# Performance work log

Measured on AMD Instinct MI355X. Metric: run time of the kernel, lower is better.

Reference implementation:

```python
import jax, jax.numpy as jnp
import numpy as np

V, D, T, H = 32000, 1024, 1024, 16
HD = D // H  # head_size = 64
B = 4


def setup_inputs() -> dict:
    key = jax.random.key(0)
    ks = jax.random.split(key, 12)
    s = 0.02
    return {
        "idx": jax.random.randint(ks[0], (B, T), 0, V),
        "tok_emb": jax.random.normal(ks[1], (V, D), jnp.float32) * s,
        "pos_emb": jax.random.normal(ks[2], (T, D), jnp.float32) * s,
        "Wq": jax.random.normal(ks[3], (H, D, HD), jnp.float32) * s,
        "Wk": jax.random.normal(ks[4], (H, D, HD), jnp.float32) * s,
        "Wv": jax.random.normal(ks[5], (H, D, HD), jnp.float32) * s,
        "W1": jax.random.normal(ks[6], (D, D), jnp.float32) * s,
        "b1": jnp.zeros((D,), jnp.float32),
        "W2": jax.random.normal(ks[7], (D, D), jnp.float32) * s,
        "b2": jnp.zeros((D,), jnp.float32),
        "Wout": jax.random.normal(ks[8], (D, V), jnp.float32) * s,
        "bout": jnp.zeros((V,), jnp.float32),
    }


def reference(idx, tok_emb, pos_emb, Wq, Wk, Wv, W1, b1, W2, b2, Wout, bout):
    t = idx.shape[1]
    x = tok_emb[idx] + pos_emb[:t]  # [B,T,D]
    # per-head q,k,v projections (no bias), vectorized over heads
    q = jnp.einsum("btd,hde->bhte", x, Wq)
    k = jnp.einsum("btd,hde->bhte", x, Wk)
    v = jnp.einsum("btd,hde->bhte", x, Wv)
    scores = jnp.einsum("bhte,bhse->bhts", q, k) / jnp.sqrt(jnp.float32(HD))
    causal = jnp.tril(jnp.ones((t, t), bool))
    scores = jnp.where(causal, scores, -jnp.inf)
    w = jax.nn.softmax(scores, axis=-1)
    att = jnp.einsum("bhts,bhse->bhte", w, v)  # [B,H,T,HD]
    # concat heads along feature dim -> [B,T,D]
    out = att.transpose(0, 2, 1, 3).reshape(idx.shape[0], t, D)
    h = jax.nn.relu(out @ W1 + b1)
    h = jax.nn.relu(h @ W2 + b2)
    logits = h @ Wout + bout  # [B,T,V]
    return logits
```

## Files before the change

kernel.cpp:

```cpp
#include <hip/hip_runtime.h>
#include <cstdint>
#include <cstddef>


#define DEV __device__ __forceinline__

typedef __attribute__((ext_vector_type(8))) short bf16x8;
typedef __attribute__((ext_vector_type(4))) float f32x4;

DEV unsigned short f2bf(float f) {
  unsigned u = __float_as_uint(f);
  u = (u + 0x7fffu + ((u >> 16) & 1u)) >> 16;
  return (unsigned short)u;
}

DEV void stage16(const void* g, void* l) {
  __builtin_amdgcn_global_load_lds(
      (const __attribute__((address_space(1))) unsigned int*)g,
      (__attribute__((address_space(3))) unsigned int*)l, 16, 0, 0);
}

__global__ __launch_bounds__(256) void k_embed(
    const int* __restrict__ idx, const float* __restrict__ tok,
    const float* __restrict__ pos, unsigned short* __restrict__ xb) {
  int i = blockIdx.x * 256 + threadIdx.x;
  int row = i >> 8;
  int c4 = i & 255;
  int t = row & 1023;
  int tokid = idx[row];
  const float4 a = ((const float4*)tok)[(size_t)tokid * 256 + c4];
  const float4 p = ((const float4*)pos)[(size_t)t * 256 + c4];
  ushort4 o;
  o.x = f2bf(a.x + p.x); o.y = f2bf(a.y + p.y);
  o.z = f2bf(a.z + p.z); o.w = f2bf(a.w + p.w);
  ((ushort4*)xb)[i] = o;
}

__global__ __launch_bounds__(256) void k_pack_qkv(
    const float* __restrict__ Wq, const float* __restrict__ Wk,
    const float* __restrict__ Wv, unsigned short* __restrict__ out) {
  __shared__ float tile[64][65];
  int blk = blockIdx.x;
  int p = blk >> 8, h = (blk >> 4) & 15, d0 = (blk & 15) * 64;
  const float* W = (p == 0) ? Wq : ((p == 1) ? Wk : Wv);
  int tid = threadIdx.x, rq = tid >> 6, cc = tid & 63;
#pragma unroll
  for (int it = 0; it < 16; ++it) {
    int dr = it * 4 + rq;
    tile[dr][cc] = W[((size_t)h * 1024 + d0 + dr) * 64 + cc];
  }
  __syncthreads();
#pragma unroll
  for (int it = 0; it < 16; ++it) {
    int e = it * 4 + rq;
    out[((size_t)(p * 1024 + h * 64 + e)) * 1024 + d0 + cc] = f2bf(tile[cc][e]);
  }
}

__global__ __launch_bounds__(256) void k_transpose(
    const float* __restrict__ in, unsigned short* __restrict__ out,
    int R, int C) {
  __shared__ float tile[64][65];
  int c0 = blockIdx.x * 64, r0 = blockIdx.y * 64;
  int tid = threadIdx.x, rq = tid >> 6, cc = tid & 63;
#pragma unroll
  for (int it = 0; it < 16; ++it) {
    int r = it * 4 + rq;
    tile[r][cc] = in[(size_t)(r0 + r) * C + c0 + cc];
  }
  __syncthreads();
#pragma unroll
  for (int it = 0; it < 16; ++it) {
    int c = it * 4 + rq;
    out[(size_t)(c0 + c) * R + r0 + cc] = f2bf(tile[cc][c]);
  }
}

template <int EP>
__global__ __launch_bounds__(256) void k_gemm(
    const unsigned short* __restrict__ A, const unsigned short* __restrict__ Bt,
    const float* __restrict__ bias, void* __restrict__ out0,
    void* __restrict__ out1, void* __restrict__ out2, int M, int N, int K) {
  __shared__ __align__(16) unsigned short As[128 * 32];
  __shared__ __align__(16) unsigned short Bs[128 * 32];
  const int tid = threadIdx.x;
  const int lane = tid & 63, w = tid >> 6;
  const int wr = w >> 1, wc = w & 1;
  const int fr = lane & 15, fg = lane >> 4;
  const int m0 = blockIdx.y * 128, n0 = blockIdx.x * 128;
  const int pch = (fg ^ ((fr >> 1) & 3)) << 3;

  f32x4 zero = {0.f, 0.f, 0.f, 0.f};
  f32x4 acc[4][4];
#pragma unroll
  for (int m = 0; m < 4; ++m)
#pragma unroll
    for (int n = 0; n < 4; ++n) acc[m][n] = zero;

  const int srow = tid >> 2;
  const int sch = (((tid & 3) ^ ((srow >> 1) & 3))) * 8;
  const unsigned short* Ab0 = A + (size_t)(m0 + srow) * K + sch;
  const unsigned short* Ab1 = A + (size_t)(m0 + 64 + srow) * K + sch;
  const unsigned short* Bb0 = Bt + (size_t)(n0 + srow) * K + sch;
  const unsigned short* Bb1 = Bt + (size_t)(n0 + 64 + srow) * K + sch;
  unsigned short* Ad0 = &As[tid * 8];
  unsigned short* Ad1 = &As[(tid + 256) * 8];
  unsigned short* Bd0 = &Bs[tid * 8];
  unsigned short* Bd1 = &Bs[(tid + 256) * 8];

  for (int k0 = 0; k0 < K; k0 += 32) {
    stage16(Ab0 + k0, Ad0);
    stage16(Ab1 + k0, Ad1);
    stage16(Bb0 + k0, Bd0);
    stage16(Bb1 + k0, Bd1);
    __syncthreads();
    bf16x8 af[4], bfv[4];
#pragma unroll
    for (int m = 0; m < 4; ++m)
      af[m] = *(const bf16x8*)&As[(wr * 64 + m * 16 + fr) * 32 + pch];
#pragma unroll
    for (int n = 0; n < 4; ++n)
      bfv[n] = *(const bf16x8*)&Bs[(wc * 64 + n * 16 + fr) * 32 + pch];
#pragma unroll
    for (int m = 0; m < 4; ++m)
#pragma unroll
      for (int n = 0; n < 4; ++n)
        acc[m][n] = __builtin_amdgcn_mfma_f32_16x16x32_bf16(af[m], bfv[n],
                                                            acc[m][n], 0, 0, 0);
    __syncthreads();
  }

#pragma unroll
  for (int m = 0; m < 4; ++m) {
#pragma unroll
    for (int n = 0; n < 4; ++n) {
      const int rb = m0 + wr * 64 + m * 16 + fg * 4;
      const int cc = n0 + wc * 64 + n * 16 + fr;
#pragma unroll
      for (int i = 0; i < 4; ++i) {
        float v = acc[m][n][i];
        const int r = rb + i;
        if (EP == 1) {
          v += bias[cc];
          v = v > 0.f ? v : 0.f;
          ((unsigned short*)out0)[(size_t)r * N + cc] = f2bf(v);
        } else if (EP == 3) {
          int p = cc >> 10, rem = cc & 1023;
          int h = rem >> 6, e = rem & 63;
          int b = r >> 10, t = r & 1023;
          unsigned short* dst =
              (p == 0) ? (unsigned short*)out0
                       : ((p == 1) ? (unsigned short*)out1 : (unsigned short*)out2);
          dst[(((size_t)(b * 16 + h) * 1024) + t) * 64 + e] = f2bf(v);
        }
      }
    }
  }
}

__global__ __launch_bounds__(512, 2) void k_gemm256(
    const unsigned short* __restrict__ A, const unsigned short* __restrict__ Bt,
    const float* __restrict__ bias, float* __restrict__ out,
    int M, int N, int K) {
  __shared__ __align__(16) unsigned short sm[4 * 16384];
  const int tid = threadIdx.x;
  const int lane = tid & 63, wid = tid >> 6;
  const int wr = wid >> 2, wc = wid & 3;
  const int fr = lane & 15, fg = lane >> 4;
  const int pch = (fg ^ ((fr >> 1) & 3)) << 3;

  const int nwg = gridDim.x * gridDim.y;
  int wg = blockIdx.y * gridDim.x + blockIdx.x;
  if ((nwg & 7) == 0) wg = (wg & 7) * (nwg >> 3) + (wg >> 3);
  const int m0 = (wg % gridDim.y) * 256;
  const int n0 = (wg / gridDim.y) * 256;

  const int srow = tid >> 2;
  const int scol = (((tid & 3) ^ ((srow >> 1) & 3))) * 8;
  const int NT = K >> 5;

#define STAGE_A(t, bb)                                                      \
  do {                                                                      \
    const unsigned short* g = A + (size_t)(m0 + srow) * K + (t) * 32 + scol; \
    stage16(g, &sm[(bb) * 16384 + tid * 8]);                                \
    stage16(g + (size_t)128 * K, &sm[(bb) * 16384 + 4096 + tid * 8]);       \
  } while (0)
#define STAGE_B(t, bb)                                                      \
  do {                                                                      \
    const unsigned short* g = Bt + (size_t)(n0 + srow) * K + (t) * 32 + scol; \
    stage16(g, &sm[(bb) * 16384 + 8192 + tid * 8]);                         \
    stage16(g + (size_t)128 * K, &sm[(bb) * 16384 + 8192 + 4096 + tid * 8]); \
  } while (0)

#define RD_G0(dA, dB, base)                                                 \
  do {                                                                      \
    _Pragma("unroll") for (int m_ = 0; m_ < 4; ++m_)                        \
      dA[m_] = *(const bf16x8*)&(base)[(wr * 128 + m_ * 16 + fr) * 32 + pch]; \
    _Pragma("unroll") for (int n_ = 0; n_ < 4; ++n_)                        \
      dB[n_] = *(const bf16x8*)&(base)[8192 + (wc * 64 + n_ * 16 + fr) * 32 + pch]; \
  } while (0)
#define RD_AHI(dA, base)                                                    \
  do {                                                                      \
    _Pragma("unroll") for (int m_ = 0; m_ < 4; ++m_)                        \
      dA[m_] = *(const bf16x8*)&(base)[(wr * 128 + (m_ + 4) * 16 + fr) * 32 + pch]; \
  } while (0)

#define MFMA_G(rbase, a, b)                                                 \
  do {                                                                      \
    __builtin_amdgcn_s_setprio(1);                                          \
    _Pragma("unroll") for (int m_ = 0; m_ < 4; ++m_)                        \
    _Pragma("unroll") for (int n_ = 0; n_ < 4; ++n_)                        \
      acc[(rbase) + m_][n_] = __builtin_amdgcn_mfma_f32_16x16x32_bf16(      \
          a[m_], b[n_], acc[(rbase) + m_][n_], 0, 0, 0);                    \
    __builtin_amdgcn_s_setprio(0);                                          \
  } while (0)

#define TILE_BODY(t, curA, curB, nxtA, nxtB)                                \
  do {                                                                      \
    const unsigned short* Ab_ = &sm[((t) & 3) * 16384];                     \
    bf16x8 a1_[4];                                                          \
    RD_AHI(a1_, Ab_);                                                       \
    if ((t) + 3 < NT) STAGE_A((t) + 3, ((t) + 3) & 3);                      \
    MFMA_G(0, curA, curB);                                                  \
    if ((t) + 1 < NT) {                                                     \
      const unsigned short* An_ = &sm[(((t) + 1) & 3) * 16384];             \
      RD_G0(nxtA, nxtB, An_);                                               \
    }                                                                       \
    if ((t) + 3 < NT) STAGE_B((t) + 3, ((t) + 3) & 3);                      \
    MFMA_G(4, a1_, curB);                                                   \
    if ((t) + 3 < NT) {                                                     \
      asm volatile("s_waitcnt vmcnt(4)" ::: "memory");                      \
    } else {                                                                \
      asm volatile("s_waitcnt vmcnt(0)" ::: "memory");                      \
    }                                                                       \
    __builtin_amdgcn_s_barrier();                                           \
  } while (0)

  f32x4 zero = {0.f, 0.f, 0.f, 0.f};
  f32x4 acc[8][4];
#pragma unroll
  for (int m = 0; m < 8; ++m)
#pragma unroll
    for (int n = 0; n < 4; ++n) acc[m][n] = zero;

  STAGE_A(0, 0); STAGE_B(0, 0);
  STAGE_A(1, 1); STAGE_B(1, 1);
  STAGE_A(2, 2); STAGE_B(2, 2);
  asm volatile("s_waitcnt vmcnt(4)" ::: "memory");
  __builtin_amdgcn_s_barrier();

  bf16x8 xA[4], xB[4], yA[4], yB[4];
  RD_G0(xA, xB, &sm[0]);

  for (int t = 0; t < NT; t += 2) {
    TILE_BODY(t, xA, xB, yA, yB);
    TILE_BODY(t + 1, yA, yB, xA, xB);
  }
#undef STAGE_A
#undef STAGE_B
#undef RD_G0
#undef RD_AHI
#undef MFMA_G
#undef TILE_BODY

#pragma unroll
  for (int m = 0; m < 8; ++m) {
#pragma unroll
    for (int n = 0; n < 4; ++n) {
      const int rb = m0 + wr * 128 + m * 16 + fg * 4;
      const int cc = n0 + wc * 64 + n * 16 + fr;
      const float bs = bias[cc];
#pragma unroll
      for (int i = 0; i < 4; ++i)
        __builtin_nontemporal_store(acc[m][n][i] + bs,
                                    &out[(size_t)(rb + i) * N + cc]);
    }
  }
}

__global__ __launch_bounds__(256) void k_attn(
    const unsigned short* __restrict__ qb, const unsigned short* __restrict__ kb,
    const unsigned short* __restrict__ vb, unsigned short* __restrict__ attx) {
  __shared__ __align__(16) unsigned short Klds[64][72];
  __shared__ __align__(16) unsigned short Vt[64][72];
  __shared__ __align__(16) unsigned short Plds[4][16][72];
  const int qt = blockIdx.x;
  const int bh = blockIdx.y;
  const int tid = threadIdx.x;
  const int w = tid >> 6, lane = tid & 63;
  const int fr = lane & 15, g = lane >> 4;
  const size_t base = (size_t)bh * (1024 * 64);
  const int q0 = qt * 64 + w * 16;
  const int q_abs = q0 + fr;

  bf16x8 qf[2];
#pragma unroll
  for (int t = 0; t < 2; ++t)
    qf[t] = *(const bf16x8*)&qb[base + (size_t)(q0 + fr) * 64 + t * 32 + g * 8];

  f32x4 zero = {0.f, 0.f, 0.f, 0.f};
  f32x4 o[4];
#pragma unroll
  for (int hb = 0; hb < 4; ++hb) o[hb] = zero;
  float m_s = -3.0e38f, l_s = 0.f;

  for (int jt = 0; jt <= qt; ++jt) {
    const int kvb = jt * 64;
#pragma unroll
    for (int it = 0; it < 2; ++it) {
      int c = tid + it * 256;
      int r = c >> 3, e0 = (c & 7) * 8;
      uint4 kd = *(const uint4*)&kb[base + (size_t)(kvb + r) * 64 + e0];
      *(uint4*)&Klds[r][e0] = kd;
      uint4 vd = *(const uint4*)&vb[base + (size_t)(kvb + r) * 64 + e0];
      const unsigned short* vs = (const unsigned short*)&vd;
#pragma unroll
      for (int j = 0; j < 8; ++j) Vt[e0 + j][r] = vs[j];
    }
    __syncthreads();

    f32x4 st[4];
#pragma unroll
    for (int f = 0; f < 4; ++f) {
      st[f] = zero;
#pragma unroll
      for (int t = 0; t < 2; ++t) {
        bf16x8 kf = *(const bf16x8*)&Klds[f * 16 + fr][t * 32 + g * 8];
        st[f] = __builtin_amdgcn_mfma_f32_16x16x32_bf16(kf, qf[t], st[f], 0, 0, 0);
      }
    }
    float sv[4][4];
    float tm = -3.0e38f;
#pragma unroll
    for (int f = 0; f < 4; ++f)
#pragma unroll
      for (int i = 0; i < 4; ++i) {
        int kv = kvb + f * 16 + g * 4 + i;
        float s = st[f][i] * 0.125f;
        if (kv > q_abs) s = -3.0e38f;
        sv[f][i] = s;
        tm = fmaxf(tm, s);
      }
    tm = fmaxf(tm, __shfl_xor(tm, 16));
    tm = fmaxf(tm, __shfl_xor(tm, 32));
    float mnew = fmaxf(m_s, tm);
    float scale = expf(m_s - mnew);
    float lsum = 0.f;
#pragma unroll
    for (int f = 0; f < 4; ++f)
#pragma unroll
      for (int i = 0; i < 4; ++i) {
        float pv = expf(sv[f][i] - mnew);
        lsum += pv;
        Plds[w][fr][f * 16 + g * 4 + i] = f2bf(pv);
      }
    lsum += __shfl_xor(lsum, 16);
    lsum += __shfl_xor(lsum, 32);
    l_s = l_s * scale + lsum;
    m_s = mnew;
#pragma unroll
    for (int i = 0; i < 4; ++i) {
      float sc = __shfl(scale, g * 4 + i);
#pragma unroll
      for (int hb = 0; hb < 4; ++hb) o[hb][i] *= sc;
    }
    __syncthreads();
#pragma unroll
    for (int t = 0; t < 2; ++t) {
      bf16x8 pf = *(const bf16x8*)&Plds[w][fr][t * 32 + g * 8];
#pragma unroll
      for (int hb = 0; hb < 4; ++hb) {
        bf16x8 vf = *(const bf16x8*)&Vt[hb * 16 + fr][t * 32 + g * 8];
        o[hb] = __builtin_amdgcn_mfma_f32_16x16x32_bf16(pf, vf, o[hb], 0, 0, 0);
      }
    }
    __syncthreads();
  }

  const float inv = 1.f / l_s;
  const int b = bh >> 4, h = bh & 15;
#pragma unroll
  for (int i = 0; i < 4; ++i) {
    float sc = __shfl(inv, g * 4 + i);
    int trow = q0 + g * 4 + i;
    size_t rowoff = ((size_t)(b * 1024 + trow)) * 1024 + h * 64;
#pragma unroll
    for (int hb = 0; hb < 4; ++hb)
      attx[rowoff + hb * 16 + fr] = f2bf(o[hb][i] * sc);
  }
}

extern "C" void kernel_launch(void* const* d_in, const int* in_sizes, int n_in,
                              void* d_out, int out_size, void* d_ws,
                              size_t ws_size, hipStream_t stream) {
  const int* idx = (const int*)d_in[0];
  const float* tok = (const float*)d_in[1];
  const float* pos = (const float*)d_in[2];
  const float* Wq = (const float*)d_in[3];
  const float* Wk = (const float*)d_in[4];
  const float* Wv = (const float*)d_in[5];
  const float* W1 = (const float*)d_in[6];
  const float* b1 = (const float*)d_in[7];
  const float* W2 = (const float*)d_in[8];
  const float* b2 = (const float*)d_in[9];
  const float* Wout = (const float*)d_in[10];
  const float* bout = (const float*)d_in[11];
  float* out = (float*)d_out;

  char* ws = (char*)d_ws;
  unsigned short* xb    = (unsigned short*)(ws + 0);
  unsigned short* wqkvT = (unsigned short*)(ws + 8388608);
  unsigned short* w1T   = (unsigned short*)(ws + 14680064);
  unsigned short* w2T   = (unsigned short*)(ws + 16777216);
  unsigned short* woutT = (unsigned short*)(ws + 18874368);
  unsigned short* qbuf  = (unsigned short*)(ws + 84410368);
  unsigned short* kbuf  = (unsigned short*)(ws + 92798976);
  unsigned short* vbuf  = (unsigned short*)(ws + 101187584);
  unsigned short* attx  = (unsigned short*)(ws + 109576192);
  unsigned short* h1    = (unsigned short*)(ws + 117964800);
  unsigned short* h2    = xb;

  k_embed<<<4096, 256, 0, stream>>>(idx, tok, pos, xb);
  k_pack_qkv<<<768, 256, 0, stream>>>(Wq, Wk, Wv, wqkvT);
  k_transpose<<<dim3(16, 16), 256, 0, stream>>>(W1, w1T, 1024, 1024);
  k_transpose<<<dim3(16, 16), 256, 0, stream>>>(W2, w2T, 1024, 1024);
  k_transpose<<<dim3(500, 16), 256, 0, stream>>>(Wout, woutT, 1024, 32000);

  k_gemm<3><<<dim3(24, 32), 256, 0, stream>>>(xb, wqkvT, nullptr, qbuf, kbuf,
                                              vbuf, 4096, 3072, 1024);
  k_attn<<<dim3(16, 64), 256, 0, stream>>>(qbuf, kbuf, vbuf, attx);
  k_gemm<1><<<dim3(8, 32), 256, 0, stream>>>(attx, w1T, b1, h1, nullptr,
                                             nullptr, 4096, 1024, 1024);
  k_gemm<1><<<dim3(8, 32), 256, 0, stream>>>(h1, w2T, b2, h2, nullptr, nullptr,
                                             4096, 1024, 1024);
  k_gemm256<<<dim3(125, 16), 512, 0, stream>>>(h2, woutT, bout, out, 4096,
                                               32000, 1024);
}
```

Baseline: 531.0 us.

## Pipeline 128-tile GEMM with multi-buffered LDS, merge transposes, coalesce output stores

New measurement: 471.4 us. -11.2%, faster.

```diff
diff --git a/kernel.cpp b/kernel.cpp
--- a/kernel.cpp
+++ b/kernel.cpp
@@ -57,11 +57,20 @@
   }
 }
 
-__global__ __launch_bounds__(256) void k_transpose(
-    const float* __restrict__ in, unsigned short* __restrict__ out,
-    int R, int C) {
+__global__ __launch_bounds__(256) void k_transpose_all(
+    const float* __restrict__ W1, const float* __restrict__ W2,
+    const float* __restrict__ Wout, unsigned short* __restrict__ w1T,
+    unsigned short* __restrict__ w2T, unsigned short* __restrict__ woutT) {
   __shared__ float tile[64][65];
-  int c0 = blockIdx.x * 64, r0 = blockIdx.y * 64;
+  int b = blockIdx.x;
+  const float* in;
+  unsigned short* outp;
+  int C, bx, by;
+  if (b < 256)      { in = W1;   outp = w1T;   C = 1024;  bx = b & 15; by = b >> 4; }
+  else if (b < 512) { b -= 256; in = W2;  outp = w2T;  C = 1024;  bx = b & 15; by = b >> 4; }
+  else              { b -= 512; in = Wout; outp = woutT; C = 32000; bx = b % 500; by = b / 500; }
+  const int R = 1024;
+  const int c0 = bx * 64, r0 = by * 64;
   int tid = threadIdx.x, rq = tid >> 6, cc = tid & 63;
 #pragma unroll
   for (int it = 0; it < 16; ++it) {
@@ -72,30 +81,27 @@
 #pragma unroll
   for (int it = 0; it < 16; ++it) {
     int c = it * 4 + rq;
-    out[(size_t)(c0 + c) * R + r0 + cc] = f2bf(tile[cc][c]);
+    outp[(size_t)(c0 + c) * R + r0 + cc] = f2bf(tile[cc][c]);
   }
 }
 
 template <int EP>
-__global__ __launch_bounds__(256) void k_gemm(
+__global__ __launch_bounds__(256, 2) void k_gemm128p(
     const unsigned short* __restrict__ A, const unsigned short* __restrict__ Bt,
     const float* __restrict__ bias, void* __restrict__ out0,
     void* __restrict__ out1, void* __restrict__ out2, int M, int N, int K) {
-  __shared__ __align__(16) unsigned short As[128 * 32];
-  __shared__ __align__(16) unsigned short Bs[128 * 32];
+  __shared__ __align__(16) unsigned short sm[4 * 8192];
   const int tid = threadIdx.x;
   const int lane = tid & 63, w = tid >> 6;
   const int wr = w >> 1, wc = w & 1;
   const int fr = lane & 15, fg = lane >> 4;
-  const int m0 = blockIdx.y * 128, n0 = blockIdx.x * 128;
   const int pch = (fg ^ ((fr >> 1) & 3)) << 3;
 
-  f32x4 zero = {0.f, 0.f, 0.f, 0.f};
-  f32x4 acc[4][4];
-#pragma unroll
-  for (int m = 0; m < 4; ++m)
-#pragma unroll
-    for (int n = 0; n < 4; ++n) acc[m][n] = zero;
+  const int nwg = gridDim.x * gridDim.y;
+  int wg = blockIdx.y * gridDim.x + blockIdx.x;
+  if ((nwg & 7) == 0) wg = (wg & 7) * (nwg >> 3) + (wg >> 3);
+  const int m0 = (wg % gridDim.y) * 128;
+  const int n0 = (wg / gridDim.y) * 128;
 
   const int srow = tid >> 2;
   const int sch = (((tid & 3) ^ ((srow >> 1) & 3))) * 8;
@@ -103,32 +109,69 @@
   const unsigned short* Ab1 = A + (size_t)(m0 + 64 + srow) * K + sch;
   const unsigned short* Bb0 = Bt + (size_t)(n0 + srow) * K + sch;
   const unsigned short* Bb1 = Bt + (size_t)(n0 + 64 + srow) * K + sch;
-  unsigned short* Ad0 = &As[tid * 8];
-  unsigned short* Ad1 = &As[(tid + 256) * 8];
-  unsigned short* Bd0 = &Bs[tid * 8];
-  unsigned short* Bd1 = &Bs[(tid + 256) * 8];
-
-  for (int k0 = 0; k0 < K; k0 += 32) {
-    stage16(Ab0 + k0, Ad0);
-    stage16(Ab1 + k0, Ad1);
-    stage16(Bb0 + k0, Bd0);
-    stage16(Bb1 + k0, Bd1);
-    __syncthreads();
-    bf16x8 af[4], bfv[4];
-#pragma unroll
-    for (int m = 0; m < 4; ++m)
-      af[m] = *(const bf16x8*)&As[(wr * 64 + m * 16 + fr) * 32 + pch];
-#pragma unroll
-    for (int n = 0; n < 4; ++n)
-      bfv[n] = *(const bf16x8*)&Bs[(wc * 64 + n * 16 + fr) * 32 + pch];
-#pragma unroll
-    for (int m = 0; m < 4; ++m)
-#pragma unroll
-      for (int n = 0; n < 4; ++n)
-        acc[m][n] = __builtin_amdgcn_mfma_f32_16x16x32_bf16(af[m], bfv[n],
-                                                            acc[m][n], 0, 0, 0);
-    __syncthreads();
-  }
+  const int NT = K >> 5;
+
+#define STAGE_T(t, bb)                                                      \
+  do {                                                                      \
+    stage16(Ab0 + (t) * 32, &sm[(bb) * 8192 + tid * 8]);                    \
+    stage16(Ab1 + (t) * 32, &sm[(bb) * 8192 + 2048 + tid * 8]);             \
+    stage16(Bb0 + (t) * 32, &sm[(bb) * 8192 + 4096 + tid * 8]);             \
+    stage16(Bb1 + (t) * 32, &sm[(bb) * 8192 + 6144 + tid * 8]);             \
+  } while (0)
+
+#define RD_ALL(dA, dB, bb)                                                  \
+  do {                                                                      \
+    const unsigned short* b_ = &sm[(bb) * 8192];                            \
+    _Pragma("unroll") for (int m_ = 0; m_ < 4; ++m_)                        \
+      dA[m_] = *(const bf16x8*)&b_[(wr * 64 + m_ * 16 + fr) * 32 + pch];    \
+    _Pragma("unroll") for (int n_ = 0; n_ < 4; ++n_)                        \
+      dB[n_] = *(const bf16x8*)&b_[4096 + (wc * 64 + n_ * 16 + fr) * 32 + pch]; \
+  } while (0)
+
+#define MFMA16(a, b)                                                        \
+  do {                                                                      \
+    __builtin_amdgcn_s_setprio(1);                                          \
+    _Pragma("unroll") for (int m_ = 0; m_ < 4; ++m_)                        \
+    _Pragma("unroll") for (int n_ = 0; n_ < 4; ++n_)                        \
+      acc[m_][n_] = __builtin_amdgcn_mfma_f32_16x16x32_bf16(                \
+          a[m_], b[n_], acc[m_][n_], 0, 0, 0);                              \
+    __builtin_amdgcn_s_setprio(0);                                          \
+  } while (0)
+
+#define TB128(t, cA, cB, nA, nB)                                            \
+  do {                                                                      \
+    if ((t) + 3 < NT) STAGE_T((t) + 3, ((t) + 3) & 3);                      \
+    if ((t) + 1 < NT) RD_ALL(nA, nB, ((t) + 1) & 3);                        \
+    MFMA16(cA, cB);                                                         \
+    if ((t) + 3 < NT) {                                                     \
+      asm volatile("s_waitcnt vmcnt(4)" ::: "memory");                      \
+    } else {                                                                \
+      asm volatile("s_waitcnt vmcnt(0)" ::: "memory");                      \
+    }                                                                       \
+    __builtin_amdgcn_s_barrier();                                           \
+  } while (0)
+
+  f32x4 zero = {0.f, 0.f, 0.f, 0.f};
+  f32x4 acc[4][4];
+#pragma unroll
+  for (int m = 0; m < 4; ++m)
+#pragma unroll
+    for (int n = 0; n < 4; ++n) acc[m][n] = zero;
+
+  STAGE_T(0, 0); STAGE_T(1, 1); STAGE_T(2, 2);
+  asm volatile("s_waitcnt vmcnt(4)" ::: "memory");
+  __builtin_amdgcn_s_barrier();
+
+  bf16x8 xA[4], xB[4], yA[4], yB[4];
+  RD_ALL(xA, xB, 0);
+  for (int t = 0; t < NT; t += 2) {
+    TB128(t, xA, xB, yA, yB);
+    TB128(t + 1, yA, yB, xA, xB);
+  }
+#undef STAGE_T
+#undef RD_ALL
+#undef MFMA16
+#undef TB128
 
 #pragma unroll
   for (int m = 0; m < 4; ++m) {
@@ -147,11 +190,11 @@
         } else if (EP == 3) {
           int p = cc >> 10, rem = cc & 1023;
           int h = rem >> 6, e = rem & 63;
-          int b = r >> 10, t = r & 1023;
+          int b = r >> 10, t2 = r & 1023;
           unsigned short* dst =
               (p == 0) ? (unsigned short*)out0
                        : ((p == 1) ? (unsigned short*)out1 : (unsigned short*)out2);
-          dst[(((size_t)(b * 16 + h) * 1024) + t) * 64 + e] = f2bf(v);
+          dst[(((size_t)(b * 16 + h) * 1024) + t2) * 64 + e] = f2bf(v);
         }
       }
     }
@@ -263,18 +306,29 @@
 #undef MFMA_G
 #undef TILE_BODY
 
-#pragma unroll
+  float* lds = (float*)sm;
+  float bsv[4];
+#pragma unroll
+  for (int n = 0; n < 4; ++n) bsv[n] = bias[n0 + wc * 64 + n * 16 + fr];
+
   for (int m = 0; m < 8; ++m) {
 #pragma unroll
     for (int n = 0; n < 4; ++n) {
-      const int rb = m0 + wr * 128 + m * 16 + fg * 4;
-      const int cc = n0 + wc * 64 + n * 16 + fr;
-      const float bs = bias[cc];
+      const int c = wc * 64 + n * 16 + fr;
 #pragma unroll
       for (int i = 0; i < 4; ++i)
-        __builtin_nontemporal_store(acc[m][n][i] + bs,
-                                    &out[(size_t)(rb + i) * N + cc]);
-    }
+        lds[(wr * 16 + fg * 4 + i) * 260 + c] = acc[m][n][i] + bsv[n];
+    }
+    __syncthreads();
+#pragma unroll
+    for (int p = 0; p < 4; ++p) {
+      const int rr = p * 8 + (tid >> 6);
+      const int c4 = (tid & 63) * 4;
+      f32x4 v = *(const f32x4*)&lds[rr * 260 + c4];
+      const int grow = m0 + ((rr < 16) ? (m * 16 + rr) : (128 + m * 16 + rr - 16));
+      __builtin_nontemporal_store(v, (f32x4*)&out[(size_t)grow * N + n0 + c4]);
+    }
+    __syncthreads();
   }
 }
 
@@ -422,17 +476,15 @@
 
   k_embed<<<4096, 256, 0, stream>>>(idx, tok, pos, xb);
   k_pack_qkv<<<768, 256, 0, stream>>>(Wq, Wk, Wv, wqkvT);
-  k_transpose<<<dim3(16, 16), 256, 0, stream>>>(W1, w1T, 1024, 1024);
-  k_transpose<<<dim3(16, 16), 256, 0, stream>>>(W2, w2T, 1024, 1024);
-  k_transpose<<<dim3(500, 16), 256, 0, stream>>>(Wout, woutT, 1024, 32000);
-
-  k_gemm<3><<<dim3(24, 32), 256, 0, stream>>>(xb, wqkvT, nullptr, qbuf, kbuf,
-                                              vbuf, 4096, 3072, 1024);
+  k_transpose_all<<<8512, 256, 0, stream>>>(W1, W2, Wout, w1T, w2T, woutT);
+
+  k_gemm128p<3><<<dim3(24, 32), 256, 0, stream>>>(xb, wqkvT, nullptr, qbuf,
+                                                  kbuf, vbuf, 4096, 3072, 1024);
   k_attn<<<dim3(16, 64), 256, 0, stream>>>(qbuf, kbuf, vbuf, attx);
-  k_gemm<1><<<dim3(8, 32), 256, 0, stream>>>(attx, w1T, b1, h1, nullptr,
-                                             nullptr, 4096, 1024, 1024);
-  k_gemm<1><<<dim3(8, 32), 256, 0, stream>>>(h1, w2T, b2, h2, nullptr, nullptr,
-                                             4096, 1024, 1024);
+  k_gemm128p<1><<<dim3(8, 32), 256, 0, stream>>>(attx, w1T, b1, h1, nullptr,
+                                                 nullptr, 4096, 1024, 1024);
+  k_gemm128p<1><<<dim3(8, 32), 256, 0, stream>>>(h1, w2T, b2, h2, nullptr,
+                                                 nullptr, 4096, 1024, 1024);
   k_gemm256<<<dim3(125, 16), 512, 0, stream>>>(h2, woutT, bout, out, 4096,
                                                32000, 1024);
 }
```
